# Kernel tuning notes

Hardware: AMD Instinct MI355X
Metric: run time of the kernel (lower is better)

The kernel has to match this reference:

```python
import jax, jax.numpy as jnp
import numpy as np

NEG_FILL = -100.0  # matches torch new_full(-100.0) init for scatter-amax


def reference(x, part_labels, parts_num=16):
    # x: (n, c, s, h, w) float; part_labels: (n, s, h, w) int in [0, parts_num)
    n, c, s, h, w = x.shape
    hw = h * w
    ns = n * s
    # (n s) c (h w)
    feat = jnp.transpose(x, (0, 2, 1, 3, 4)).reshape(ns, c, hw)
    labels = part_labels.reshape(ns, hw).astype(jnp.int32)

    b3 = jnp.arange(ns)[:, None, None]          # (ns,1,1)
    ch = jnp.arange(c)[None, :, None]            # (1,c,1)
    lbl3 = labels[:, None, :]                    # (ns,1,hw) -> broadcasts to (ns,c,hw)

    pooled_sum = jnp.zeros((ns, c, parts_num), x.dtype).at[b3, ch, lbl3].add(feat)
    b2 = jnp.arange(ns)[:, None]
    pooled_count = jnp.zeros((ns, parts_num), x.dtype).at[b2, labels].add(1.0)  # (ns,P)
    pooled_max = jnp.full((ns, c, parts_num), NEG_FILL, x.dtype).at[b3, ch, lbl3].max(feat)

    count = pooled_count[:, None, :]             # (ns,1,P)
    pooled_mean = pooled_sum / jnp.maximum(count, 1.0)
    pooled_max = jnp.where(count > 0, pooled_max, 0.0)
    pooled = pooled_mean + pooled_max            # (ns,c,P)
    # (n s) c p -> n c s p
    return jnp.transpose(pooled.reshape(n, s, c, parts_num), (0, 2, 1, 3))


def setup_inputs() -> dict:
    key = jax.random.key(0)
    k1, k2 = jax.random.split(key)
    n, c, s, h, w = 16, 256, 32, 16, 11
    parts_num = 16
    x = jax.random.normal(k1, (n, c, s, h, w), dtype=jnp.float32)
    part_labels = jax.random.randint(k2, (n, s, h, w), 0, parts_num, dtype=jnp.int64)
    return {"x": x, "part_labels": part_labels, "parts_num": parts_num}
```

## Files before the change

### kernel.cpp

```cpp
#include <hip/hip_runtime.h>


constexpr int C   = 256;
constexpr int S   = 32;
constexpr int HW  = 176;
constexpr int P   = 16;
constexpr int ROW = S * HW;
constexpr int REC = 256;
constexpr float NEG_FILL = -100.0f;

__global__ __launch_bounds__(256) void prep_kernel(const int* __restrict__ labels,
                                                   unsigned char* __restrict__ ws)
{
    __shared__ int cnt[P], off[P];
    __shared__ unsigned char rec[REC];
    const int tid = threadIdx.x, ns = blockIdx.x;

    int lab = 0, r = 0;
    if (tid < HW) lab = labels[(size_t)ns * HW + tid];
    if (tid < P) cnt[tid] = 0;
    __syncthreads();
    if (tid < HW) r = atomicAdd(&cnt[lab], 1);
    __syncthreads();
    if (tid == 0) {
        int run = 0;
        #pragma unroll
        for (int p = 0; p < P; ++p) { off[p] = run; run += (cnt[p] + 3) & ~3; }
    }
    __syncthreads();
    if (tid < HW) rec[off[lab] + r] = (unsigned char)tid;
    if (tid < P) {
        rec[224 + tid] = (unsigned char)cnt[tid];
        rec[240 + tid] = (unsigned char)off[tid];
    }
    __syncthreads();
    if (tid < REC / 4)
        ((unsigned*)(ws + (size_t)ns * REC))[tid] = ((const unsigned*)rec)[tid];
}

__device__ __forceinline__ void gload_lds16(const void* g, void* l) {
    __builtin_amdgcn_global_load_lds(
        (const __attribute__((address_space(1))) void*)g,
        (__attribute__((address_space(3))) void*)l, 16, 0, 0);
}

__global__ __launch_bounds__(256) void hpp_main(const float* __restrict__ x,
                                                const unsigned char* __restrict__ ws,
                                                float* __restrict__ out)
{
    __shared__ float         tile[ROW];
    __shared__ unsigned char meta[S * REC];

    const int tid = threadIdx.x;
    const int blk = blockIdx.x;
    const int n   = blk >> 8;

    const float*         xb = x  + (size_t)blk * ROW;
    const unsigned char* mb = ws + (size_t)n * (S * REC);

    #pragma unroll
    for (int i = 0; i < 2; ++i)
        gload_lds16((const uint4*)mb + i * 256 + tid,
                    (uint4*)meta + i * 256 + tid);
    #pragma unroll
    for (int i = 0; i < 5; ++i)
        gload_lds16((const float4*)xb + i * 256 + tid,
                    (float4*)tile + i * 256 + tid);
    if (tid < 128)
        gload_lds16((const float4*)xb + 5 * 256 + tid,
                    (float4*)tile + 5 * 256 + tid);

    __syncthreads();

    const int p   = tid & 15;
    const int sh  = tid >> 4;

    #pragma unroll
    for (int q = 0; q < 2; ++q) {
        const int s = sh + 16 * q;
        const unsigned char* rec = &meta[s * REC];
        const int k    = rec[224 + p];
        const int base = rec[240 + p];
        const float*    tc = &tile[s * HW];
        const unsigned* pw = (const unsigned*)(rec + base);

        unsigned w0 = pw[0], w1 = pw[1], w2 = pw[2], w3 = pw[3];

        float a0 = 0.f, a1 = 0.f, m0 = NEG_FILL, m1 = NEG_FILL;
        #define CH(w, jb)                                                  \
            do { if (k > (jb)) {                                           \
                float b0 = tc[(w) & 0xFF];                                 \
                float b1 = tc[((w) >> 8) & 0xFF];                          \
                float b2 = tc[((w) >> 16) & 0xFF];                         \
                float b3 = tc[(w) >> 24];                                  \
                a0 += b0; m0 = fmaxf(m0, b0);                              \
                if (k > (jb) + 1) { a1 += b1; m1 = fmaxf(m1, b1); }        \
                if (k > (jb) + 2) { a0 += b2; m0 = fmaxf(m0, b2); }        \
                if (k > (jb) + 3) { a1 += b3; m1 = fmaxf(m1, b3); }        \
            } } while (0)
        CH(w0, 0); CH(w1, 4); CH(w2, 8); CH(w3, 12);
        for (int j = 16; j < k; j += 4) {
            unsigned w = pw[j >> 2];
            CH(w, j);
        }
        #undef CH

        float res = (k > 0) ? (a0 + a1) / (float)k + fmaxf(m0, m1) : 0.f;
        out[((size_t)blk * S + s) * P + p] = res;
    }
}

__global__ void hpp_naive(const float* __restrict__ x,
                          const int* __restrict__ labels,
                          float* __restrict__ out)
{
    int t = blockIdx.x * 256 + threadIdx.x;
    int p = t & 15, c = (t >> 4) & 255, ns = t >> 12;
    int n = ns >> 5, s = ns & 31;
    const int*   ln  = labels + (size_t)ns * HW;
    const float* row = x + ((size_t)(n * C + c) * S + s) * HW;
    float sum = 0.f, mx = NEG_FILL; int k = 0;
    for (int i = 0; i < HW; ++i)
        if (ln[i] == p) { float v = row[i]; sum += v; mx = fmaxf(mx, v); k++; }
    out[((size_t)(n * C + c) * S + s) * P + p] = k ? sum / (float)k + mx : 0.f;
}

extern "C" void kernel_launch(void* const* d_in, const int* in_sizes, int n_in,
                              void* d_out, int out_size, void* d_ws, size_t ws_size,
                              hipStream_t stream) {
    const float* x      = (const float*)d_in[0];
    const int*   labels = (const int*)d_in[1];
    float*       out    = (float*)d_out;

    const int ns_total = in_sizes[1] / HW;
    const size_t need  = (size_t)ns_total * REC;

    if (ws_size >= need) {
        prep_kernel<<<ns_total, 256, 0, stream>>>(labels, (unsigned char*)d_ws);
        hpp_main<<<ns_total / S * C, 256, 0, stream>>>(x, (const unsigned char*)d_ws, out);
    } else {
        hpp_naive<<<(out_size + 255) / 256, 256, 0, stream>>>(x, labels, out);
    }
}
```

Baseline: 138.9 us.

## Retile pooling kernel to per-(n, channel-group, s) blocks with padded LDS rows

```diff
diff --git a/kernel.cpp b/kernel.cpp
--- a/kernel.cpp
+++ b/kernel.cpp
@@ -6,6 +6,8 @@
 constexpr int HW  = 176;
 constexpr int P   = 16;
 constexpr int ROW = S * HW;
+constexpr int GC  = 16;
+constexpr int PITCH = 180;
 constexpr int REC = 256;
 constexpr float NEG_FILL = -100.0f;
 
@@ -18,7 +20,8 @@
 
     int lab = 0, r = 0;
     if (tid < HW) lab = labels[(size_t)ns * HW + tid];
-    if (tid < P) cnt[tid] = 0;
+    if (tid < P)  cnt[tid] = 0;
+    if (tid < 56) ((unsigned*)rec)[tid] = 0u;
     __syncthreads();
     if (tid < HW) r = atomicAdd(&cnt[lab], 1);
     __syncthreads();
@@ -48,66 +51,62 @@
                                                 const unsigned char* __restrict__ ws,
                                                 float* __restrict__ out)
 {
-    __shared__ float         tile[ROW];
-    __shared__ unsigned char meta[S * REC];
+    __shared__ float         tile[GC * PITCH];
+    __shared__ unsigned char rec[REC];
 
     const int tid = threadIdx.x;
     const int blk = blockIdx.x;
-    const int n   = blk >> 8;
+    const int s   = blk & 31;
+    const int t2  = blk >> 5;
+    const int cg  = t2 & 15;
+    const int n   = t2 >> 4;
+    const int ns  = (n << 5) | s;
 
-    const float*         xb = x  + (size_t)blk * ROW;
-    const unsigned char* mb = ws + (size_t)n * (S * REC);
+    const int lane = tid & 63, wv = tid >> 6;
 
-    #pragma unroll
-    for (int i = 0; i < 2; ++i)
-        gload_lds16((const uint4*)mb + i * 256 + tid,
-                    (uint4*)meta + i * 256 + tid);
-    #pragma unroll
-    for (int i = 0; i < 5; ++i)
-        gload_lds16((const float4*)xb + i * 256 + tid,
-                    (float4*)tile + i * 256 + tid);
-    if (tid < 128)
-        gload_lds16((const float4*)xb + 5 * 256 + tid,
-                    (float4*)tile + 5 * 256 + tid);
+    if (tid < 16)
+        gload_lds16((const uint4*)(ws + (size_t)ns * REC) + tid, rec);
 
+    const float* xb = x + (size_t)(n * C + cg * GC) * ROW + s * HW;
+    if (lane < 44) {
+        #pragma unroll
+        for (int r = 0; r < 4; ++r) {
+            const int row = wv * 4 + r;
+            gload_lds16((const float4*)(xb + (size_t)row * ROW) + lane,
+                        &tile[row * PITCH]);
+        }
+    }
     __syncthreads();
 
-    const int p   = tid & 15;
-    const int sh  = tid >> 4;
+    const int p = tid >> 4, c = tid & 15;
+    const int k    = rec[224 + p];
+    const int base = rec[240 + p];
+    const unsigned* pw = (const unsigned*)(rec + base);
+    const float*    tc = &tile[c * PITCH];
 
-    #pragma unroll
-    for (int q = 0; q < 2; ++q) {
-        const int s = sh + 16 * q;
-        const unsigned char* rec = &meta[s * REC];
-        const int k    = rec[224 + p];
-        const int base = rec[240 + p];
-        const float*    tc = &tile[s * HW];
-        const unsigned* pw = (const unsigned*)(rec + base);
+    unsigned w0 = pw[0], w1 = pw[1], w2 = pw[2], w3 = pw[3];
 
-        unsigned w0 = pw[0], w1 = pw[1], w2 = pw[2], w3 = pw[3];
+    float a0 = 0.f, a1 = 0.f, m0 = NEG_FILL, m1 = NEG_FILL;
+    #define CH(w, jb)                                                  \
+        do { if (k > (jb)) {                                           \
+            float b0 = tc[(w) & 0xFF];                                 \
+            float b1 = tc[((w) >> 8) & 0xFF];                          \
+            float b2 = tc[((w) >> 16) & 0xFF];                         \
+            float b3 = tc[(w) >> 24];                                  \
+            a0 += b0; m0 = fmaxf(m0, b0);                              \
+            if (k > (jb) + 1) { a1 += b1; m1 = fmaxf(m1, b1); }        \
+            if (k > (jb) + 2) { a0 += b2; m0 = fmaxf(m0, b2); }        \
+            if (k > (jb) + 3) { a1 += b3; m1 = fmaxf(m1, b3); }        \
+        } } while (0)
+    CH(w0, 0); CH(w1, 4); CH(w2, 8); CH(w3, 12);
+    for (int j = 16; j < k; j += 4) {
+        unsigned w = pw[j >> 2];
+        CH(w, j);
+    }
+    #undef CH
 
-        float a0 = 0.f, a1 = 0.f, m0 = NEG_FILL, m1 = NEG_FILL;
-        #define CH(w, jb)                                                  \
-            do { if (k > (jb)) {                                           \
-                float b0 = tc[(w) & 0xFF];                                 \
-                float b1 = tc[((w) >> 8) & 0xFF];                          \
-                float b2 = tc[((w) >> 16) & 0xFF];                         \
-                float b3 = tc[(w) >> 24];                                  \
-                a0 += b0; m0 = fmaxf(m0, b0);                              \
-                if (k > (jb) + 1) { a1 += b1; m1 = fmaxf(m1, b1); }        \
-                if (k > (jb) + 2) { a0 += b2; m0 = fmaxf(m0, b2); }        \
-                if (k > (jb) + 3) { a1 += b3; m1 = fmaxf(m1, b3); }        \
-            } } while (0)
-        CH(w0, 0); CH(w1, 4); CH(w2, 8); CH(w3, 12);
-        for (int j = 16; j < k; j += 4) {
-            unsigned w = pw[j >> 2];
-            CH(w, j);
-        }
-        #undef CH
-
-        float res = (k > 0) ? (a0 + a1) / (float)k + fmaxf(m0, m1) : 0.f;
-        out[((size_t)blk * S + s) * P + p] = res;
-    }
+    float res = (k > 0) ? (a0 + a1) / (float)k + fmaxf(m0, m1) : 0.f;
+    out[((size_t)(n * C + cg * GC + c) * S + s) * P + p] = res;
 }
 
 __global__ void hpp_naive(const float* __restrict__ x,
@@ -137,7 +136,8 @@
 
     if (ws_size >= need) {
         prep_kernel<<<ns_total, 256, 0, stream>>>(labels, (unsigned char*)d_ws);
-        hpp_main<<<ns_total / S * C, 256, 0, stream>>>(x, (const unsigned char*)d_ws, out);
+        hpp_main<<<ns_total * (C / GC), 256, 0, stream>>>(
+            x, (const unsigned char*)d_ws, out);
     } else {
         hpp_naive<<<(out_size + 255) / 256, 256, 0, stream>>>(x, labels, out);
     }
```

After: 140.5 us. About the same (+1.1%).
